# Performance work log

Measured on AMD Instinct MI355X. Metric: run time of the kernel, lower is better.

## Reference

```python
import jax, jax.numpy as jnp
import numpy as np

B, H, W, DIM, NH, HD = 2, 64, 160, 256, 8, 32
R0, R1 = 1, 1                      # win_r (x, y)
WX, WY = 2 * R0 + 2, 2 * R1 + 2    # window extents
A = WX * WY                        # attn_num = 16
SCALE = HD ** (-0.5)


def setup_inputs() -> dict:
    key = jax.random.key(0)
    ks = jax.random.split(key, 6)
    x = jax.random.normal(ks[0], (B, H, W, DIM), jnp.float32)
    # float match positions anywhere in the image; clamp in reference() keeps windows in-bounds
    u = jax.random.uniform(ks[1], (B, H * W, 2), jnp.float32)
    max_offset = u * jnp.array([W, H], jnp.float32)
    Wq = jax.random.normal(ks[2], (DIM, NH * HD), jnp.float32) * 0.02
    Wk = jax.random.normal(ks[3], (DIM, NH * HD), jnp.float32) * 0.02
    Wv = jax.random.normal(ks[4], (DIM, NH * HD), jnp.float32) * 0.02
    Wproj = jax.random.normal(ks[5], (NH * HD, DIM), jnp.float32) * 0.02
    return dict(x=x, max_offset=max_offset, Wq=Wq, Wk=Wk, Wv=Wv, Wproj=Wproj)


def reference(x, max_offset, Wq, Wk, Wv, Wproj):
    b, h, w, _ = x.shape
    n = h * w
    xf = x.reshape(b, n, -1)
    q = (xf @ Wq).reshape(b, n, NH, HD)
    k = (xf @ Wk).reshape(b, n, NH, HD)
    v = (xf @ Wv).reshape(b, n, NH, HD)

    # clamp_max_offset: keep the (2r+2)^2 window fully inside the image
    ox = jnp.clip(max_offset[..., 0], R0, w - 1 - R0 - 0.001)
    oy = jnp.clip(max_offset[..., 1], R1, h - 1 - R1 - 0.001)
    mx, my = jnp.floor(ox), jnp.floor(oy)
    fx, fy = ox - mx, oy - my  # bilinear fractions

    # window gather indices: rows my-R1..my+R1+1, cols mx-R0..mx+R0+1
    ix = mx.astype(jnp.int32)[..., None] + jnp.arange(-R0, R0 + 2)  # (b,n,WX)
    iy = my.astype(jnp.int32)[..., None] + jnp.arange(-R1, R1 + 2)  # (b,n,WY)
    idx = (iy[:, :, :, None] * w + ix[:, :, None, :]).reshape(b, n, A)  # (b,n,A)

    gather = jax.vmap(lambda t, i: t[i])  # per-batch row gather
    kg = gather(k.reshape(b, n, NH * HD), idx).reshape(b, n, A, NH, HD)
    vg = gather(v.reshape(b, n, NH * HD), idx).reshape(b, n, A, NH, HD)

    attn = jnp.einsum('bnhd,bnahd->bnha', q, kg) * SCALE  # (b,n,NH,A)

    # bilinear weights: edge elements weighted by (1-f)/f, interior by 1
    wx = jnp.concatenate([(1 - fx)[..., None], jnp.ones((b, n, 2 * R0), fx.dtype), fx[..., None]], axis=-1)
    wy = jnp.concatenate([(1 - fy)[..., None], jnp.ones((b, n, 2 * R1), fy.dtype), fy[..., None]], axis=-1)
    bw = (wy[:, :, :, None] * wx[:, :, None, :]).reshape(b, n, 1, A)

    # bilinear-weighted stable softmax
    m = jnp.max(attn, axis=-1, keepdims=True)
    e = jnp.exp(attn - m) * bw
    p = e / jnp.sum(e, axis=-1, keepdims=True)

    out = jnp.einsum('bnha,bnahd->bnhd', p, vg).reshape(b, n, NH * HD)
    out = out @ Wproj
    return out.reshape(b, h, w, -1)
```

## Files before the change

### kernel.cpp

```cpp
#include <hip/hip_runtime.h>
#include <math.h>

#define Bb   2
#define Hh   64
#define Ww   160
#define DIMc 256
#define Nn   (Hh * Ww)
#define SCALEf 0.17677669529663687f

typedef unsigned short u16;
typedef unsigned int   u32;
typedef __bf16 bf16x8 __attribute__((ext_vector_type(8)));
typedef float  f32x4  __attribute__((ext_vector_type(4)));

__device__ __forceinline__ u16 f2bf(float f) {
    u32 u = __float_as_uint(f);
    u += 0x7fffu + ((u >> 16) & 1u);
    return (u16)(u >> 16);
}
__device__ __forceinline__ u32 pack2(float lo, float hi) {
    return (u32)f2bf(lo) | ((u32)f2bf(hi) << 16);
}
__device__ __forceinline__ float bflo(u32 u) { return __uint_as_float(u << 16); }
__device__ __forceinline__ float bfhi(u32 u) { return __uint_as_float(u & 0xffff0000u); }

__global__ __launch_bounds__(256) void prep(const float* __restrict__ x,
                                            const float* __restrict__ Wq,
                                            const float* __restrict__ Wk,
                                            const float* __restrict__ Wv,
                                            const float* __restrict__ Wp,
                                            u16* __restrict__ xb,
                                            u16* __restrict__ WtAll)
{
    const int bid = blockIdx.x;
    if (bid < 5120) {
        size_t id = (size_t)bid * 256 + threadIdx.x;
        float4 vv = *(const float4*)(x + id * 4);
        ushort4 ov = make_ushort4(f2bf(vv.x), f2bf(vv.y), f2bf(vv.z), f2bf(vv.w));
        *(ushort4*)(xb + id * 4) = ov;
    } else {
        int id = (bid - 5120) * 256 + threadIdx.x;
        int wsel = id >> 16;
        int rem  = id & 65535;
        int kk = rem >> 8, nn = rem & 255;
        const float* W = (wsel == 0) ? Wq : (wsel == 1) ? Wk : (wsel == 2) ? Wv : Wp;
        WtAll[(size_t)wsel * 65536 + nn * 256 + kk] = f2bf(W[kk * 256 + nn]);
    }
}

template <bool BF16OUT>
__device__ __forceinline__ void gemm_core(const u16* __restrict__ Ag,
                                          const u16* __restrict__ Btg,
                                          u16* __restrict__ Cb,
                                          float* __restrict__ Cf)
{
    __shared__ u16 sA[128 * 32];
    __shared__ u16 sB[128 * 32];

    const int t    = threadIdx.x;
    const int lane = t & 63;
    const int wv   = t >> 6;
    const int wm   = wv & 1;
    const int wn   = wv >> 1;
    const int m0   = blockIdx.y * 128;
    const int n0   = blockIdx.x * 128;

    const int r0  = t >> 2;
    const int kc0 = (t & 3) * 8;

    const int col  = lane & 15;
    const int quad = lane >> 4;

    f32x4 acc[4][4];
#pragma unroll
    for (int i = 0; i < 4; ++i)
#pragma unroll
        for (int j = 0; j < 4; ++j)
            acc[i][j] = (f32x4){0.f, 0.f, 0.f, 0.f};

    const u16* Abase = Ag + (size_t)m0 * 256;
    const u16* Bbase = Btg + (size_t)n0 * 256;

    for (int k0 = 0; k0 < 256; k0 += 32) {
        uint4 a0 = *(const uint4*)(Abase + (size_t)r0 * 256 + k0 + kc0);
        uint4 a1 = *(const uint4*)(Abase + (size_t)(64 + r0) * 256 + k0 + kc0);
        uint4 b0 = *(const uint4*)(Bbase + (size_t)r0 * 256 + k0 + kc0);
        uint4 b1 = *(const uint4*)(Bbase + (size_t)(64 + r0) * 256 + k0 + kc0);
        __syncthreads();
        *(uint4*)(sA + r0 * 32 + kc0)        = a0;
        *(uint4*)(sA + (64 + r0) * 32 + kc0) = a1;
        *(uint4*)(sB + r0 * 32 + kc0)        = b0;
        *(uint4*)(sB + (64 + r0) * 32 + kc0) = b1;
        __syncthreads();

        bf16x8 af[4], bfr[4];
#pragma unroll
        for (int mt = 0; mt < 4; ++mt)
            af[mt] = *(const bf16x8*)(sA + (wm * 64 + mt * 16 + col) * 32 + quad * 8);
#pragma unroll
        for (int nt = 0; nt < 4; ++nt)
            bfr[nt] = *(const bf16x8*)(sB + (wn * 64 + nt * 16 + col) * 32 + quad * 8);

#pragma unroll
        for (int mt = 0; mt < 4; ++mt)
#pragma unroll
            for (int nt = 0; nt < 4; ++nt)
                acc[mt][nt] = __builtin_amdgcn_mfma_f32_16x16x32_bf16(af[mt], bfr[nt], acc[mt][nt], 0, 0, 0);
    }

#pragma unroll
    for (int mt = 0; mt < 4; ++mt) {
#pragma unroll
        for (int nt = 0; nt < 4; ++nt) {
            const int rowb = m0 + wm * 64 + mt * 16 + quad * 4;
            const int colg = n0 + wn * 64 + nt * 16 + col;
#pragma unroll
            for (int rr = 0; rr < 4; ++rr) {
                float val = acc[mt][nt][rr];
                if (BF16OUT) Cb[(size_t)(rowb + rr) * 256 + colg] = f2bf(val);
                else         Cf[(size_t)(rowb + rr) * 256 + colg] = val;
            }
        }
    }
}

__global__ __launch_bounds__(256) void gemm_qkv(const u16* __restrict__ xb,
                                                const u16* __restrict__ WtAll,
                                                u16* __restrict__ q,
                                                u16* __restrict__ k,
                                                u16* __restrict__ v)
{
    const int z = blockIdx.z;
    u16* C = (z == 0) ? q : (z == 1) ? k : v;
    gemm_core<true>(xb, WtAll + (size_t)z * 65536, C, nullptr);
}

__global__ __launch_bounds__(256) void gemm_proj(const u16* __restrict__ ao,
                                                 const u16* __restrict__ WtAll,
                                                 float* __restrict__ out)
{
    gemm_core<false>(ao, WtAll + (size_t)3 * 65536, nullptr, out);
}

__global__ __launch_bounds__(256) void attn_kernel(const u16* __restrict__ q,
                                                   const u16* __restrict__ k,
                                                   const u16* __restrict__ v,
                                                   const float* __restrict__ moff,
                                                   u16* __restrict__ ao)
{
    const int wv   = threadIdx.x >> 6;
    const int lane = threadIdx.x & 63;
    const int pos  = blockIdx.x * 4 + wv;
    const int rowbase = (pos >= Nn) ? Nn : 0;

    float2 mo = *(const float2*)(moff + (size_t)pos * 2);
    float ox = fminf(fmaxf(mo.x, 1.0f), (float)(Ww - 2) - 0.001f);
    float oy = fminf(fmaxf(mo.y, 1.0f), (float)(Hh - 2) - 0.001f);
    float mxf = floorf(ox), myf = floorf(oy);
    float fx = ox - mxf, fy = oy - myf;
    int imx = (int)mxf, imy = (int)myf;

    const int h  = lane & 7;
    const int a0 = lane >> 3;

    uint4 q4[4];
    {
        const uint4* qp = (const uint4*)(q + (size_t)pos * 256 + h * 32);
#pragma unroll
        for (int jj = 0; jj < 4; ++jj) q4[jj] = qp[jj];
    }

    float s[2];
#pragma unroll
    for (int p = 0; p < 2; ++p) {
        int a   = a0 + 8 * p;
        int row = rowbase + (imy + (a >> 2) - 1) * Ww + imx + (a & 3) - 1;
        const uint4* kp = (const uint4*)(k + (size_t)row * 256 + h * 32);
        float acc = 0.f;
#pragma unroll
        for (int jj = 0; jj < 4; ++jj) {
            uint4 kw = kp[jj];
            acc += bflo(q4[jj].x) * bflo(kw.x) + bfhi(q4[jj].x) * bfhi(kw.x)
                 + bflo(q4[jj].y) * bflo(kw.y) + bfhi(q4[jj].y) * bfhi(kw.y)
                 + bflo(q4[jj].z) * bflo(kw.z) + bfhi(q4[jj].z) * bfhi(kw.z)
                 + bflo(q4[jj].w) * bflo(kw.w) + bfhi(q4[jj].w) * bfhi(kw.w);
        }
        s[p] = acc * SCALEf;
    }

    auto wc = [](int r, float f) { return r == 0 ? 1.f - f : (r == 3 ? f : 1.f); };
    float bw0 = wc(a0 >> 2, fy) * wc(a0 & 3, fx);
    float bw1 = wc((a0 + 8) >> 2, fy) * wc(a0 & 3, fx);

    float m = fmaxf(s[0], s[1]);
    m = fmaxf(m, __shfl_xor(m, 8));
    m = fmaxf(m, __shfl_xor(m, 16));
    m = fmaxf(m, __shfl_xor(m, 32));
    float e0 = expf(s[0] - m) * bw0;
    float e1 = expf(s[1] - m) * bw1;
    float sum = e0 + e1;
    sum += __shfl_xor(sum, 8);
    sum += __shfl_xor(sum, 16);
    sum += __shfl_xor(sum, 32);
    float inv = 1.f / sum;
    float p0 = e0 * inv, p1 = e1 * inv;

    float acc0 = 0.f, acc1 = 0.f, acc2 = 0.f, acc3 = 0.f;
    const int myh = lane >> 3;
#pragma unroll
    for (int a = 0; a < 16; ++a) {
        int row = rowbase + (imy + (a >> 2) - 1) * Ww + imx + (a & 3) - 1;
        uint2 vw = *(const uint2*)(v + (size_t)row * 256 + 4 * lane);
        int src = ((a & 7) << 3) | myh;
        float pa = __shfl(a < 8 ? p0 : p1, src);
        acc0 += pa * bflo(vw.x); acc1 += pa * bfhi(vw.x);
        acc2 += pa * bflo(vw.y); acc3 += pa * bfhi(vw.y);
    }
    uint2 o;
    o.x = pack2(acc0, acc1);
    o.y = pack2(acc2, acc3);
    *(uint2*)(ao + (size_t)pos * 256 + 4 * lane) = o;
}

extern "C" void kernel_launch(void* const* d_in, const int* in_sizes, int n_in,
                              void* d_out, int out_size, void* d_ws, size_t ws_size,
                              hipStream_t stream)
{
    const float* x     = (const float*)d_in[0];
    const float* moff  = (const float*)d_in[1];
    const float* Wq    = (const float*)d_in[2];
    const float* Wk    = (const float*)d_in[3];
    const float* Wv    = (const float*)d_in[4];
    const float* Wproj = (const float*)d_in[5];
    float* out = (float*)d_out;

    const size_t NTOT = (size_t)Bb * Nn * DIMc;
    u16* ws    = (u16*)d_ws;
    u16* xb    = ws;
    u16* WtAll = xb + NTOT;
    u16* q     = WtAll + 4 * 65536;
    u16* k     = q + NTOT;
    u16* v     = k + NTOT;
    u16* ao    = v + NTOT;

    prep<<<dim3(6144), dim3(256), 0, stream>>>(x, Wq, Wk, Wv, Wproj, xb, WtAll);
    gemm_qkv<<<dim3(2, 160, 3), dim3(256), 0, stream>>>(xb, WtAll, q, k, v);
    attn_kernel<<<dim3(Bb * Nn / 4), dim3(256), 0, stream>>>(q, k, v, moff, ao);
    gemm_proj<<<dim3(2, 160, 1), dim3(256), 0, stream>>>(ao, WtAll, out);
}
```

Before: 146.2 us.

## Fuse x fp32-to-bf16 conversion into QKV GEMM and retile to 64x256

Drops the separate pass that converts x to bf16 and instead converts fp32 x on the fly while loading the A tile in the QKV GEMM. The GEMM tile changes from 128x128 to 64 rows by the full 256 columns, so each block covers all output columns and A is read once per projection. The prep kernel now only transposes and converts weights. This removes one full read and write of x through global memory, but each block now reloads the whole 256x256 weight slice per k-step and stages twice as much fp32 A data per load.

```diff
diff --git a/kernel.cpp b/kernel.cpp
--- a/kernel.cpp
+++ b/kernel.cpp
@@ -24,53 +24,39 @@
 __device__ __forceinline__ float bflo(u32 u) { return __uint_as_float(u << 16); }
 __device__ __forceinline__ float bfhi(u32 u) { return __uint_as_float(u & 0xffff0000u); }
 
-__global__ __launch_bounds__(256) void prep(const float* __restrict__ x,
-                                            const float* __restrict__ Wq,
-                                            const float* __restrict__ Wk,
-                                            const float* __restrict__ Wv,
-                                            const float* __restrict__ Wp,
-                                            u16* __restrict__ xb,
-                                            u16* __restrict__ WtAll)
-{
-    const int bid = blockIdx.x;
-    if (bid < 5120) {
-        size_t id = (size_t)bid * 256 + threadIdx.x;
-        float4 vv = *(const float4*)(x + id * 4);
-        ushort4 ov = make_ushort4(f2bf(vv.x), f2bf(vv.y), f2bf(vv.z), f2bf(vv.w));
-        *(ushort4*)(xb + id * 4) = ov;
-    } else {
-        int id = (bid - 5120) * 256 + threadIdx.x;
-        int wsel = id >> 16;
-        int rem  = id & 65535;
-        int kk = rem >> 8, nn = rem & 255;
-        const float* W = (wsel == 0) ? Wq : (wsel == 1) ? Wk : (wsel == 2) ? Wv : Wp;
-        WtAll[(size_t)wsel * 65536 + nn * 256 + kk] = f2bf(W[kk * 256 + nn]);
-    }
-}
-
-template <bool BF16OUT>
-__device__ __forceinline__ void gemm_core(const u16* __restrict__ Ag,
-                                          const u16* __restrict__ Btg,
-                                          u16* __restrict__ Cb,
-                                          float* __restrict__ Cf)
-{
-    __shared__ u16 sA[128 * 32];
-    __shared__ u16 sB[128 * 32];
+__global__ __launch_bounds__(256) void prep_w(const float* __restrict__ Wq,
+                                              const float* __restrict__ Wk,
+                                              const float* __restrict__ Wv,
+                                              const float* __restrict__ Wp,
+                                              u16* __restrict__ WtAll)
+{
+    int id = blockIdx.x * 256 + threadIdx.x;
+    int wsel = id >> 16;
+    int rem  = id & 65535;
+    int kk = rem >> 8, nn = rem & 255;
+    const float* W = (wsel == 0) ? Wq : (wsel == 1) ? Wk : (wsel == 2) ? Wv : Wp;
+    WtAll[(size_t)wsel * 65536 + nn * 256 + kk] = f2bf(W[kk * 256 + nn]);
+}
+
+template <bool A_IS_F32, bool BF16OUT>
+__device__ __forceinline__ void gemm_core64(const void* __restrict__ Avoid,
+                                            const u16* __restrict__ Btg,
+                                            u16* __restrict__ Cb,
+                                            float* __restrict__ Cf,
+                                            int m0)
+{
+    __shared__ u16 sA[64 * 32];
+    __shared__ u16 sB[256 * 32];
 
     const int t    = threadIdx.x;
     const int lane = t & 63;
     const int wv   = t >> 6;
-    const int wm   = wv & 1;
-    const int wn   = wv >> 1;
-    const int m0   = blockIdx.y * 128;
-    const int n0   = blockIdx.x * 128;
+    const int col  = lane & 15;
+    const int quad = lane >> 4;
 
     const int r0  = t >> 2;
     const int kc0 = (t & 3) * 8;
 
-    const int col  = lane & 15;
-    const int quad = lane >> 4;
-
     f32x4 acc[4][4];
 #pragma unroll
     for (int i = 0; i < 4; ++i)
@@ -78,28 +64,44 @@
         for (int j = 0; j < 4; ++j)
             acc[i][j] = (f32x4){0.f, 0.f, 0.f, 0.f};
 
-    const u16* Abase = Ag + (size_t)m0 * 256;
-    const u16* Bbase = Btg + (size_t)n0 * 256;
+    const float* Af = (const float*)Avoid;
+    const u16*   Ab = (const u16*)Avoid;
 
     for (int k0 = 0; k0 < 256; k0 += 32) {
-        uint4 a0 = *(const uint4*)(Abase + (size_t)r0 * 256 + k0 + kc0);
-        uint4 a1 = *(const uint4*)(Abase + (size_t)(64 + r0) * 256 + k0 + kc0);
-        uint4 b0 = *(const uint4*)(Bbase + (size_t)r0 * 256 + k0 + kc0);
-        uint4 b1 = *(const uint4*)(Bbase + (size_t)(64 + r0) * 256 + k0 + kc0);
+        uint4 areg;
+        if (A_IS_F32) {
+            const float* ap = Af + (size_t)(m0 + r0) * 256 + k0 + kc0;
+            float4 a0 = *(const float4*)ap;
+            float4 a1 = *(const float4*)(ap + 4);
+            areg.x = pack2(a0.x, a0.y);
+            areg.y = pack2(a0.z, a0.w);
+            areg.z = pack2(a1.x, a1.y);
+            areg.w = pack2(a1.z, a1.w);
+        } else {
+            areg = *(const uint4*)(Ab + (size_t)(m0 + r0) * 256 + k0 + kc0);
+        }
+        uint4 breg[4];
+#pragma unroll
+        for (int i = 0; i < 4; ++i) {
+            int c = i * 256 + t, rB = c >> 2, kcB = (c & 3) * 8;
+            breg[i] = *(const uint4*)(Btg + (size_t)rB * 256 + k0 + kcB);
+        }
         __syncthreads();
-        *(uint4*)(sA + r0 * 32 + kc0)        = a0;
-        *(uint4*)(sA + (64 + r0) * 32 + kc0) = a1;
-        *(uint4*)(sB + r0 * 32 + kc0)        = b0;
-        *(uint4*)(sB + (64 + r0) * 32 + kc0) = b1;
+        *(uint4*)(sA + r0 * 32 + kc0) = areg;
+#pragma unroll
+        for (int i = 0; i < 4; ++i) {
+            int c = i * 256 + t, rB = c >> 2, kcB = (c & 3) * 8;
+            *(uint4*)(sB + rB * 32 + kcB) = breg[i];
+        }
         __syncthreads();
 
         bf16x8 af[4], bfr[4];
 #pragma unroll
         for (int mt = 0; mt < 4; ++mt)
-            af[mt] = *(const bf16x8*)(sA + (wm * 64 + mt * 16 + col) * 32 + quad * 8);
+            af[mt] = *(const bf16x8*)(sA + (mt * 16 + col) * 32 + quad * 8);
 #pragma unroll
         for (int nt = 0; nt < 4; ++nt)
-            bfr[nt] = *(const bf16x8*)(sB + (wn * 64 + nt * 16 + col) * 32 + quad * 8);
+            bfr[nt] = *(const bf16x8*)(sB + (wv * 64 + nt * 16 + col) * 32 + quad * 8);
 
 #pragma unroll
         for (int mt = 0; mt < 4; ++mt)
@@ -112,8 +114,8 @@
     for (int mt = 0; mt < 4; ++mt) {
 #pragma unroll
         for (int nt = 0; nt < 4; ++nt) {
-            const int rowb = m0 + wm * 64 + mt * 16 + quad * 4;
-            const int colg = n0 + wn * 64 + nt * 16 + col;
+            const int rowb = m0 + mt * 16 + quad * 4;
+            const int colg = wv * 64 + nt * 16 + col;
 #pragma unroll
             for (int rr = 0; rr < 4; ++rr) {
                 float val = acc[mt][nt][rr];
@@ -124,22 +126,22 @@
     }
 }
 
-__global__ __launch_bounds__(256) void gemm_qkv(const u16* __restrict__ xb,
+__global__ __launch_bounds__(256) void gemm_qkv(const float* __restrict__ x,
                                                 const u16* __restrict__ WtAll,
                                                 u16* __restrict__ q,
                                                 u16* __restrict__ k,
                                                 u16* __restrict__ v)
 {
-    const int z = blockIdx.z;
+    const int z = blockIdx.y;
     u16* C = (z == 0) ? q : (z == 1) ? k : v;
-    gemm_core<true>(xb, WtAll + (size_t)z * 65536, C, nullptr);
+    gemm_core64<true, true>(x, WtAll + (size_t)z * 65536, C, nullptr, blockIdx.x * 64);
 }
 
 __global__ __launch_bounds__(256) void gemm_proj(const u16* __restrict__ ao,
                                                  const u16* __restrict__ WtAll,
                                                  float* __restrict__ out)
 {
-    gemm_core<false>(ao, WtAll + (size_t)3 * 65536, nullptr, out);
+    gemm_core64<false, false>(ao, WtAll + (size_t)3 * 65536, nullptr, out, blockIdx.x * 64);
 }
 
 __global__ __launch_bounds__(256) void attn_kernel(const u16* __restrict__ q,
@@ -236,15 +238,14 @@
 
     const size_t NTOT = (size_t)Bb * Nn * DIMc;
     u16* ws    = (u16*)d_ws;
-    u16* xb    = ws;
-    u16* WtAll = xb + NTOT;
+    u16* WtAll = ws;
     u16* q     = WtAll + 4 * 65536;
     u16* k     = q + NTOT;
     u16* v     = k + NTOT;
     u16* ao    = v + NTOT;
 
-    prep<<<dim3(6144), dim3(256), 0, stream>>>(x, Wq, Wk, Wv, Wproj, xb, WtAll);
-    gemm_qkv<<<dim3(2, 160, 3), dim3(256), 0, stream>>>(xb, WtAll, q, k, v);
+    prep_w<<<dim3(1024), dim3(256), 0, stream>>>(Wq, Wk, Wv, Wproj, WtAll);
+    gemm_qkv<<<dim3(320, 3), dim3(256), 0, stream>>>(x, WtAll, q, k, v);
     attn_kernel<<<dim3(Bb * Nn / 4), dim3(256), 0, stream>>>(q, k, v, moff, ao);
-    gemm_proj<<<dim3(2, 160, 1), dim3(256), 0, stream>>>(ao, WtAll, out);
-}
+    gemm_proj<<<dim3(320), dim3(256), 0, stream>>>(ao, WtAll, out);
+}
```

New measurement: 198.6 us. 1.36x slower.

## Keep weight fragments in registers and stream A directly in GEMMs

Applied to the files above, without the earlier changes.

Restructures both GEMMs so each block owns a 64-row strip across all 256 output columns. Each wave preloads its 64-column slice of the transposed weight into registers once, then streams A fragments straight from global memory with no LDS staging and no per-k barriers. The bf16 QKV output is staged through a 32 KB LDS tile so global stores are coalesced 16-byte writes. This removes shared-memory round trips and synchronisation in the K loop, but costs heavy register use (128 VGPRs for B) and relies on uncoalesced, cache-dependent A loads.

```diff
diff --git a/kernel.cpp b/kernel.cpp
--- a/kernel.cpp
+++ b/kernel.cpp
@@ -23,6 +23,10 @@
 }
 __device__ __forceinline__ float bflo(u32 u) { return __uint_as_float(u << 16); }
 __device__ __forceinline__ float bfhi(u32 u) { return __uint_as_float(u & 0xffff0000u); }
+
+__device__ __forceinline__ bf16x8 as_bf8(uint4 u) {
+    union { uint4 u; bf16x8 b; } c; c.u = u; return c.b;
+}
 
 __global__ __launch_bounds__(256) void prep(const float* __restrict__ x,
                                             const float* __restrict__ Wq,
@@ -49,27 +53,25 @@
 }
 
 template <bool BF16OUT>
-__device__ __forceinline__ void gemm_core(const u16* __restrict__ Ag,
-                                          const u16* __restrict__ Btg,
-                                          u16* __restrict__ Cb,
-                                          float* __restrict__ Cf)
-{
-    __shared__ u16 sA[128 * 32];
-    __shared__ u16 sB[128 * 32];
-
+__device__ __forceinline__ void gemm_ws(const u16* __restrict__ Ag,
+                                        const u16* __restrict__ Btg,
+                                        u16* __restrict__ Cb,
+                                        float* __restrict__ Cf,
+                                        int m0)
+{
     const int t    = threadIdx.x;
     const int lane = t & 63;
     const int wv   = t >> 6;
-    const int wm   = wv & 1;
-    const int wn   = wv >> 1;
-    const int m0   = blockIdx.y * 128;
-    const int n0   = blockIdx.x * 128;
-
-    const int r0  = t >> 2;
-    const int kc0 = (t & 3) * 8;
-
     const int col  = lane & 15;
     const int quad = lane >> 4;
+    const int nb   = wv * 64;
+
+    uint4 breg[4][8];
+#pragma unroll
+    for (int nt = 0; nt < 4; ++nt)
+#pragma unroll
+        for (int kf = 0; kf < 8; ++kf)
+            breg[nt][kf] = *(const uint4*)(Btg + (size_t)(nb + nt * 16 + col) * 256 + kf * 32 + quad * 8);
 
     f32x4 acc[4][4];
 #pragma unroll
@@ -79,67 +81,68 @@
             acc[i][j] = (f32x4){0.f, 0.f, 0.f, 0.f};
 
     const u16* Abase = Ag + (size_t)m0 * 256;
-    const u16* Bbase = Btg + (size_t)n0 * 256;
-
-    for (int k0 = 0; k0 < 256; k0 += 32) {
-        uint4 a0 = *(const uint4*)(Abase + (size_t)r0 * 256 + k0 + kc0);
-        uint4 a1 = *(const uint4*)(Abase + (size_t)(64 + r0) * 256 + k0 + kc0);
-        uint4 b0 = *(const uint4*)(Bbase + (size_t)r0 * 256 + k0 + kc0);
-        uint4 b1 = *(const uint4*)(Bbase + (size_t)(64 + r0) * 256 + k0 + kc0);
+
+#pragma unroll
+    for (int kf = 0; kf < 8; ++kf) {
+        uint4 areg[4];
+#pragma unroll
+        for (int mt = 0; mt < 4; ++mt)
+            areg[mt] = *(const uint4*)(Abase + (size_t)(mt * 16 + col) * 256 + kf * 32 + quad * 8);
+#pragma unroll
+        for (int mt = 0; mt < 4; ++mt)
+#pragma unroll
+            for (int nt = 0; nt < 4; ++nt)
+                acc[mt][nt] = __builtin_amdgcn_mfma_f32_16x16x32_bf16(
+                    as_bf8(areg[mt]), as_bf8(breg[nt][kf]), acc[mt][nt], 0, 0, 0);
+    }
+
+    if constexpr (BF16OUT) {
+        __shared__ u16 sC[64 * 256];
+#pragma unroll
+        for (int mt = 0; mt < 4; ++mt)
+#pragma unroll
+            for (int nt = 0; nt < 4; ++nt)
+#pragma unroll
+                for (int rr = 0; rr < 4; ++rr)
+                    sC[(mt * 16 + quad * 4 + rr) * 256 + nb + nt * 16 + col] = f2bf(acc[mt][nt][rr]);
         __syncthreads();
-        *(uint4*)(sA + r0 * 32 + kc0)        = a0;
-        *(uint4*)(sA + (64 + r0) * 32 + kc0) = a1;
-        *(uint4*)(sB + r0 * 32 + kc0)        = b0;
-        *(uint4*)(sB + (64 + r0) * 32 + kc0) = b1;
-        __syncthreads();
-
-        bf16x8 af[4], bfr[4];
-#pragma unroll
-        for (int mt = 0; mt < 4; ++mt)
-            af[mt] = *(const bf16x8*)(sA + (wm * 64 + mt * 16 + col) * 32 + quad * 8);
-#pragma unroll
-        for (int nt = 0; nt < 4; ++nt)
-            bfr[nt] = *(const bf16x8*)(sB + (wn * 64 + nt * 16 + col) * 32 + quad * 8);
-
-#pragma unroll
-        for (int mt = 0; mt < 4; ++mt)
-#pragma unroll
-            for (int nt = 0; nt < 4; ++nt)
-                acc[mt][nt] = __builtin_amdgcn_mfma_f32_16x16x32_bf16(af[mt], bfr[nt], acc[mt][nt], 0, 0, 0);
-    }
-
-#pragma unroll
-    for (int mt = 0; mt < 4; ++mt) {
-#pragma unroll
-        for (int nt = 0; nt < 4; ++nt) {
-            const int rowb = m0 + wm * 64 + mt * 16 + quad * 4;
-            const int colg = n0 + wn * 64 + nt * 16 + col;
-#pragma unroll
-            for (int rr = 0; rr < 4; ++rr) {
-                float val = acc[mt][nt][rr];
-                if (BF16OUT) Cb[(size_t)(rowb + rr) * 256 + colg] = f2bf(val);
-                else         Cf[(size_t)(rowb + rr) * 256 + colg] = val;
+#pragma unroll
+        for (int i = 0; i < 8; ++i) {
+            int j   = i * 256 + t;
+            int row = j >> 5;
+            int off = (j & 31) * 8;
+            *(uint4*)(Cb + (size_t)(m0 + row) * 256 + off) = *(const uint4*)(sC + row * 256 + off);
+        }
+    } else {
+#pragma unroll
+        for (int mt = 0; mt < 4; ++mt)
+#pragma unroll
+            for (int nt = 0; nt < 4; ++nt) {
+                const int rowb = m0 + mt * 16 + quad * 4;
+                const int colg = nb + nt * 16 + col;
+#pragma unroll
+                for (int rr = 0; rr < 4; ++rr)
+                    Cf[(size_t)(rowb + rr) * 256 + colg] = acc[mt][nt][rr];
             }
-        }
-    }
-}
-
-__global__ __launch_bounds__(256) void gemm_qkv(const u16* __restrict__ xb,
-                                                const u16* __restrict__ WtAll,
-                                                u16* __restrict__ q,
-                                                u16* __restrict__ k,
-                                                u16* __restrict__ v)
-{
-    const int z = blockIdx.z;
+    }
+}
+
+__global__ __launch_bounds__(256, 2) void gemm_qkv(const u16* __restrict__ xb,
+                                                   const u16* __restrict__ WtAll,
+                                                   u16* __restrict__ q,
+                                                   u16* __restrict__ k,
+                                                   u16* __restrict__ v)
+{
+    const int z = blockIdx.x;
     u16* C = (z == 0) ? q : (z == 1) ? k : v;
-    gemm_core<true>(xb, WtAll + (size_t)z * 65536, C, nullptr);
-}
-
-__global__ __launch_bounds__(256) void gemm_proj(const u16* __restrict__ ao,
-                                                 const u16* __restrict__ WtAll,
-                                                 float* __restrict__ out)
-{
-    gemm_core<false>(ao, WtAll + (size_t)3 * 65536, nullptr, out);
+    gemm_ws<true>(xb, WtAll + (size_t)z * 65536, C, nullptr, blockIdx.y * 64);
+}
+
+__global__ __launch_bounds__(256, 2) void gemm_proj(const u16* __restrict__ ao,
+                                                    const u16* __restrict__ WtAll,
+                                                    float* __restrict__ out)
+{
+    gemm_ws<false>(ao, WtAll + (size_t)3 * 65536, nullptr, out, blockIdx.x * 64);
 }
 
 __global__ __launch_bounds__(256) void attn_kernel(const u16* __restrict__ q,
@@ -244,7 +247,7 @@
     u16* ao    = v + NTOT;
 
     prep<<<dim3(6144), dim3(256), 0, stream>>>(x, Wq, Wk, Wv, Wproj, xb, WtAll);
-    gemm_qkv<<<dim3(2, 160, 3), dim3(256), 0, stream>>>(xb, WtAll, q, k, v);
+    gemm_qkv<<<dim3(3, 320), dim3(256), 0, stream>>>(xb, WtAll, q, k, v);
     attn_kernel<<<dim3(Bb * Nn / 4), dim3(256), 0, stream>>>(q, k, v, moff, ao);
-    gemm_proj<<<dim3(2, 160, 1), dim3(256), 0, stream>>>(ao, WtAll, out);
-}
+    gemm_proj<<<dim3(320), dim3(256), 0, stream>>>(ao, WtAll, out);
+}
```

After: 170.4 us. +16.5%, slower.

## Fuse x bf16 conversion into QKV GEMM and stage GEMM epilogue through LDS

Applied to the files above, without the earlier changes.

The separate x-to-bf16 conversion pass is removed: the QKV GEMM now reads fp32 x directly and converts to bf16 while loading tiles, so prep only transposes and converts the weights. Both GEMM epilogues now write accumulators to shared memory first and then store coalesced 16-byte vectors to global memory, instead of scattered 2- or 4-byte stores. The goal is to save one full read and write of the activation tensor and to make output stores coalesced. In exchange, x is read in fp32 (twice the bytes) by each of the 6 N-tile/z blocks, and the epilogue adds extra barriers and uses 32KB of LDS.

```diff
diff --git a/kernel.cpp b/kernel.cpp
--- a/kernel.cpp
+++ b/kernel.cpp
@@ -24,38 +24,29 @@
 __device__ __forceinline__ float bflo(u32 u) { return __uint_as_float(u << 16); }
 __device__ __forceinline__ float bfhi(u32 u) { return __uint_as_float(u & 0xffff0000u); }
 
-__global__ __launch_bounds__(256) void prep(const float* __restrict__ x,
-                                            const float* __restrict__ Wq,
-                                            const float* __restrict__ Wk,
-                                            const float* __restrict__ Wv,
-                                            const float* __restrict__ Wp,
-                                            u16* __restrict__ xb,
-                                            u16* __restrict__ WtAll)
-{
-    const int bid = blockIdx.x;
-    if (bid < 5120) {
-        size_t id = (size_t)bid * 256 + threadIdx.x;
-        float4 vv = *(const float4*)(x + id * 4);
-        ushort4 ov = make_ushort4(f2bf(vv.x), f2bf(vv.y), f2bf(vv.z), f2bf(vv.w));
-        *(ushort4*)(xb + id * 4) = ov;
-    } else {
-        int id = (bid - 5120) * 256 + threadIdx.x;
-        int wsel = id >> 16;
-        int rem  = id & 65535;
-        int kk = rem >> 8, nn = rem & 255;
-        const float* W = (wsel == 0) ? Wq : (wsel == 1) ? Wk : (wsel == 2) ? Wv : Wp;
-        WtAll[(size_t)wsel * 65536 + nn * 256 + kk] = f2bf(W[kk * 256 + nn]);
-    }
-}
-
-template <bool BF16OUT>
-__device__ __forceinline__ void gemm_core(const u16* __restrict__ Ag,
+__global__ __launch_bounds__(256) void prep_w(const float* __restrict__ Wq,
+                                              const float* __restrict__ Wk,
+                                              const float* __restrict__ Wv,
+                                              const float* __restrict__ Wp,
+                                              u16* __restrict__ WtAll)
+{
+    int id = blockIdx.x * 256 + threadIdx.x;
+    int wsel = id >> 16;
+    int rem  = id & 65535;
+    int kk = rem >> 8, nn = rem & 255;
+    const float* W = (wsel == 0) ? Wq : (wsel == 1) ? Wk : (wsel == 2) ? Wv : Wp;
+    WtAll[(size_t)wsel * 65536 + nn * 256 + kk] = f2bf(W[kk * 256 + nn]);
+}
+
+template <bool A_IS_F32, bool BF16OUT>
+__device__ __forceinline__ void gemm_core(const void* __restrict__ Avoid,
                                           const u16* __restrict__ Btg,
                                           u16* __restrict__ Cb,
                                           float* __restrict__ Cf)
 {
-    __shared__ u16 sA[128 * 32];
-    __shared__ u16 sB[128 * 32];
+    __shared__ __align__(16) char smem[32768];
+    u16* sA = (u16*)smem;
+    u16* sB = (u16*)(smem + 8192);
 
     const int t    = threadIdx.x;
     const int lane = t & 63;
@@ -78,12 +69,25 @@
         for (int j = 0; j < 4; ++j)
             acc[i][j] = (f32x4){0.f, 0.f, 0.f, 0.f};
 
-    const u16* Abase = Ag + (size_t)m0 * 256;
-    const u16* Bbase = Btg + (size_t)n0 * 256;
+    const float* Af = (const float*)Avoid;
+    const u16*   Ab = (const u16*)Avoid;
+    const u16*   Bbase = Btg + (size_t)n0 * 256;
 
     for (int k0 = 0; k0 < 256; k0 += 32) {
-        uint4 a0 = *(const uint4*)(Abase + (size_t)r0 * 256 + k0 + kc0);
-        uint4 a1 = *(const uint4*)(Abase + (size_t)(64 + r0) * 256 + k0 + kc0);
+        uint4 a0, a1;
+        if (A_IS_F32) {
+            const float* ap0 = Af + (size_t)(m0 + r0) * 256 + k0 + kc0;
+            const float* ap1 = Af + (size_t)(m0 + 64 + r0) * 256 + k0 + kc0;
+            float4 f0 = *(const float4*)ap0, f1 = *(const float4*)(ap0 + 4);
+            float4 f2 = *(const float4*)ap1, f3 = *(const float4*)(ap1 + 4);
+            a0.x = pack2(f0.x, f0.y); a0.y = pack2(f0.z, f0.w);
+            a0.z = pack2(f1.x, f1.y); a0.w = pack2(f1.z, f1.w);
+            a1.x = pack2(f2.x, f2.y); a1.y = pack2(f2.z, f2.w);
+            a1.z = pack2(f3.x, f3.y); a1.w = pack2(f3.z, f3.w);
+        } else {
+            a0 = *(const uint4*)(Ab + (size_t)(m0 + r0) * 256 + k0 + kc0);
+            a1 = *(const uint4*)(Ab + (size_t)(m0 + 64 + r0) * 256 + k0 + kc0);
+        }
         uint4 b0 = *(const uint4*)(Bbase + (size_t)r0 * 256 + k0 + kc0);
         uint4 b1 = *(const uint4*)(Bbase + (size_t)(64 + r0) * 256 + k0 + kc0);
         __syncthreads();
@@ -108,23 +112,58 @@
                 acc[mt][nt] = __builtin_amdgcn_mfma_f32_16x16x32_bf16(af[mt], bfr[nt], acc[mt][nt], 0, 0, 0);
     }
 
-#pragma unroll
-    for (int mt = 0; mt < 4; ++mt) {
-#pragma unroll
-        for (int nt = 0; nt < 4; ++nt) {
-            const int rowb = m0 + wm * 64 + mt * 16 + quad * 4;
-            const int colg = n0 + wn * 64 + nt * 16 + col;
-#pragma unroll
-            for (int rr = 0; rr < 4; ++rr) {
-                float val = acc[mt][nt][rr];
-                if (BF16OUT) Cb[(size_t)(rowb + rr) * 256 + colg] = f2bf(val);
-                else         Cf[(size_t)(rowb + rr) * 256 + colg] = val;
+    __syncthreads();
+    if (BF16OUT) {
+        u16* sC = (u16*)smem;
+#pragma unroll
+        for (int mt = 0; mt < 4; ++mt)
+#pragma unroll
+            for (int nt = 0; nt < 4; ++nt) {
+                const int rw = wm * 64 + mt * 16 + quad * 4;
+                const int cl = wn * 64 + nt * 16 + col;
+#pragma unroll
+                for (int rr = 0; rr < 4; ++rr)
+                    sC[(rw + rr) * 128 + cl] = f2bf(acc[mt][nt][rr]);
             }
-        }
-    }
-}
-
-__global__ __launch_bounds__(256) void gemm_qkv(const u16* __restrict__ xb,
+        __syncthreads();
+#pragma unroll
+        for (int i = 0; i < 8; ++i) {
+            int j   = i * 256 + t;
+            int row = j >> 4;
+            int off = (j & 15) * 8;
+            *(uint4*)(Cb + (size_t)(m0 + row) * 256 + n0 + off) = *(const uint4*)(sC + row * 128 + off);
+        }
+    } else {
+        float* sC = (float*)smem;
+#pragma unroll
+        for (int ph = 0; ph < 2; ++ph) {
+            if (wm == ph) {
+#pragma unroll
+                for (int mt = 0; mt < 4; ++mt)
+#pragma unroll
+                    for (int nt = 0; nt < 4; ++nt) {
+                        const int rw = mt * 16 + quad * 4;
+                        const int cl = wn * 64 + nt * 16 + col;
+#pragma unroll
+                        for (int rr = 0; rr < 4; ++rr)
+                            sC[(rw + rr) * 128 + cl] = acc[mt][nt][rr];
+                    }
+            }
+            __syncthreads();
+#pragma unroll
+            for (int i = 0; i < 8; ++i) {
+                int j   = i * 256 + t;
+                int row = j >> 5;
+                int off = (j & 31) * 4;
+                *(float4*)(Cf + (size_t)(m0 + ph * 64 + row) * 256 + n0 + off) =
+                    *(const float4*)(sC + row * 128 + off);
+            }
+            __syncthreads();
+        }
+    }
+}
+
+__global__ __launch_bounds__(256) void gemm_qkv(const float* __restrict__ x,
                                                 const u16* __restrict__ WtAll,
                                                 u16* __restrict__ q,
                                                 u16* __restrict__ k,
@@ -132,14 +171,14 @@
 {
     const int z = blockIdx.z;
     u16* C = (z == 0) ? q : (z == 1) ? k : v;
-    gemm_core<true>(xb, WtAll + (size_t)z * 65536, C, nullptr);
+    gemm_core<true, true>(x, WtAll + (size_t)z * 65536, C, nullptr);
 }
 
 __global__ __launch_bounds__(256) void gemm_proj(const u16* __restrict__ ao,
                                                  const u16* __restrict__ WtAll,
                                                  float* __restrict__ out)
 {
-    gemm_core<false>(ao, WtAll + (size_t)3 * 65536, nullptr, out);
+    gemm_core<false, false>(ao, WtAll + (size_t)3 * 65536, nullptr, out);
 }
 
 __global__ __launch_bounds__(256) void attn_kernel(const u16* __restrict__ q,
@@ -236,15 +275,14 @@
 
     const size_t NTOT = (size_t)Bb * Nn * DIMc;
     u16* ws    = (u16*)d_ws;
-    u16* xb    = ws;
-    u16* WtAll = xb + NTOT;
+    u16* WtAll = ws;
     u16* q     = WtAll + 4 * 65536;
     u16* k     = q + NTOT;
     u16* v     = k + NTOT;
     u16* ao    = v + NTOT;
 
-    prep<<<dim3(6144), dim3(256), 0, stream>>>(x, Wq, Wk, Wv, Wproj, xb, WtAll);
-    gemm_qkv<<<dim3(2, 160, 3), dim3(256), 0, stream>>>(xb, WtAll, q, k, v);
+    prep_w<<<dim3(1024), dim3(256), 0, stream>>>(Wq, Wk, Wv, Wproj, WtAll);
+    gemm_qkv<<<dim3(2, 160, 3), dim3(256), 0, stream>>>(x, WtAll, q, k, v);
     attn_kernel<<<dim3(Bb * Nn / 4), dim3(256), 0, stream>>>(q, k, v, moff, ao);
     gemm_proj<<<dim3(2, 160, 1), dim3(256), 0, stream>>>(ao, WtAll, out);
 }
```

Result: no change. 143.8 us (median of 2 runs) (-1.6%).
